# Kernel optimization log

Hardware: AMD Instinct MI355X
Metric: run time of the kernel (lower is better)

Reference implementation:

```python
import jax, jax.numpy as jnp
import numpy as np
from jax import lax

B, N, CIN, COUT, FPS, K, TCH, M, H = 8, 4096, 128, 256, 1024, 24, 256, 32, 4
HD = TCH // H
BN_SCALE = 1.0 / np.sqrt(1.0 + 1e-5)  # eval-mode BN: running_mean=0, running_var=1


def _gather(points, idx):
    # points [B,N,C], idx [B,S] or [B,S,K] -> gathered points
    return jax.vmap(lambda p, i: p[i])(points, idx)


def _bn(x, g, b):
    return x * (g * BN_SCALE) + b


def _ln(x, g, b):
    mu = jnp.mean(x, -1, keepdims=True)
    v = jnp.var(x, -1, keepdims=True)
    return (x - mu) / jnp.sqrt(v + 1e-5) * g + b


def _gelu(x):
    return jax.nn.gelu(x, approximate=False)


def _fps(xyz, npoint, farthest0):
    Bb, Nn, _ = xyz.shape
    def step(carry, _):
        dmin, far = carry
        c = jax.vmap(lambda p, i: p[i])(xyz, far)  # [B,3]
        d = jnp.sum((xyz - c[:, None, :]) ** 2, -1)
        dmin = jnp.minimum(dmin, d)
        return (dmin, jnp.argmax(dmin, -1)), far
    init = (jnp.full((Bb, Nn), 1e10, xyz.dtype), farthest0)
    _, cents = lax.scan(step, init, None, length=npoint)
    return cents.T  # [B, npoint]


def _sqdist(src, dst):
    d = -2.0 * jnp.einsum('bnc,bmc->bnm', src, dst)
    d = d + jnp.sum(src ** 2, -1)[:, :, None]
    d = d + jnp.sum(dst ** 2, -1)[:, None, :]
    return d


def _forward(xyz, x, t, farthest0, Wproj, gproj, bproj, Wl1, gl1, bl1, Wl2, gl2, bl2,
             Wc1, gc1, bc1, Wc2, gc2, bc2, Wq, Wk, Wv, Wo,
             ln1g, ln1b, Wqkv, Wao, ln2g, ln2b, Wf1, Wf2):
    # --- GenerateGraph: FPS + KNN grouping ---
    fps_idx = _fps(xyz, FPS, farthest0)            # [B,S]
    new_xyz = _gather(xyz, fps_idx)                # [B,S,3]
    xT = jnp.transpose(x, (0, 2, 1))               # [B,N,Cin]
    new_pts = _gather(xT, fps_idx)                 # [B,S,Cin]
    dist = _sqdist(new_xyz, xyz)                   # [B,S,N]
    _, idx = lax.top_k(-dist, K)                   # [B,S,K] nearest neighbors
    grouped = _gather(xT, idx)                     # [B,S,K,Cin]
    edge = grouped - new_pts[:, :, None, :]
    # --- Local: Conv1DBR proj + Conv1DBRRes (channels-last, 1x1 convs = GEMM) ---
    h = _gelu(_bn(jnp.einsum('bskc,oc->bsko', edge, Wproj), gproj, bproj))
    r = _gelu(_bn(jnp.einsum('bsko,po->bskp', h, Wl1), gl1, bl1))
    r = _bn(jnp.einsum('bskp,op->bsko', r, Wl2), gl2, bl2)
    h = _gelu(r + h)
    f = jnp.max(h, axis=2)                         # adaptive_max_pool over k -> [B,S,O]
    # --- Channel (ca): Conv1DBRRes on centroid features ---
    r = _gelu(_bn(f @ Wc1.T, gc1, bc1))
    r = _bn(r @ Wc2.T, gc2, bc2)
    f = _gelu(r + f)
    x_out = jnp.transpose(f, (0, 2, 1))            # [B,O,S]
    # --- Local2Former: tokens attend to local features ---
    q = t @ Wq.T
    kk = f @ Wk.T
    v = f @ Wv.T
    a = jax.nn.softmax(jnp.einsum('bmd,bsd->bms', q, kk) * (TCH ** -0.5), axis=-1)
    t = t + jnp.einsum('bms,bsd->bmd', a, v) @ Wo.T
    # --- Former: one pre-norm encoder layer (MHA + MLP) ---
    hn = _ln(t, ln1g, ln1b)
    qkv = (hn @ Wqkv.T).reshape(B, M, 3, H, HD).transpose(2, 0, 3, 1, 4)
    qh, kh, vh = qkv[0], qkv[1], qkv[2]            # [B,H,M,hd]
    attn = jax.nn.softmax(jnp.einsum('bhmd,bhnd->bhmn', qh, kh) * (HD ** -0.5), axis=-1)
    o = jnp.einsum('bhmn,bhnd->bhmd', attn, vh).transpose(0, 2, 1, 3).reshape(B, M, TCH)
    t = t + o @ Wao.T
    hn = _ln(t, ln2g, ln2b)
    t = t + _gelu(hn @ Wf1.T) @ Wf2.T
    return new_xyz, x_out, t


def setup_inputs() -> dict:
    key = jax.random.key(0)
    ks = jax.random.split(key, 40)
    def w(k, o, i):
        return jax.random.normal(k, (o, i), jnp.float32) / np.sqrt(i)
    def g(k, c):
        return 1.0 + 0.1 * jax.random.normal(k, (c,), jnp.float32)
    def bta(k, c):
        return 0.1 * jax.random.normal(k, (c,), jnp.float32)
    inp = {
        'xyz': jax.random.normal(ks[0], (B, N, 3), jnp.float32),
        'x': jax.random.normal(ks[1], (B, CIN, N), jnp.float32),
        't': jax.random.normal(ks[2], (B, M, TCH), jnp.float32),
        'farthest0': jax.random.randint(ks[3], (B,), 0, N),
        'Wproj': w(ks[4], COUT, CIN), 'gproj': g(ks[5], COUT), 'bproj': bta(ks[6], COUT),
        'Wl1': w(ks[7], COUT, COUT), 'gl1': g(ks[8], COUT), 'bl1': bta(ks[9], COUT),
        'Wl2': w(ks[10], COUT, COUT), 'gl2': g(ks[11], COUT), 'bl2': bta(ks[12], COUT),
        'Wc1': w(ks[13], COUT, COUT), 'gc1': g(ks[14], COUT), 'bc1': bta(ks[15], COUT),
        'Wc2': w(ks[16], COUT, COUT), 'gc2': g(ks[17], COUT), 'bc2': bta(ks[18], COUT),
        'Wq': w(ks[19], TCH, TCH), 'Wk': w(ks[20], TCH, COUT), 'Wv': w(ks[21], TCH, COUT),
        'Wo': w(ks[22], TCH, TCH),
        'ln1g': g(ks[23], TCH), 'ln1b': bta(ks[24], TCH),
        'Wqkv': w(ks[25], 3 * TCH, TCH), 'Wao': w(ks[26], TCH, TCH),
        'ln2g': g(ks[27], TCH), 'ln2b': bta(ks[28], TCH),
        'Wf1': w(ks[29], 2 * TCH, TCH), 'Wf2': w(ks[30], TCH, 2 * TCH),
    }
    return inp


def reference(xyz, x, t, farthest0, Wproj, gproj, bproj, Wl1, gl1, bl1, Wl2, gl2, bl2,
              Wc1, gc1, bc1, Wc2, gc2, bc2, Wq, Wk, Wv, Wo,
              ln1g, ln1b, Wqkv, Wao, ln2g, ln2b, Wf1, Wf2):
    return _forward(xyz, x, t, farthest0, Wproj, gproj, bproj, Wl1, gl1, bl1, Wl2, gl2, bl2,
                    Wc1, gc1, bc1, Wc2, gc2, bc2, Wq, Wk, Wv, Wo,
                    ln1g, ln1b, Wqkv, Wao, ln2g, ln2b, Wf1, Wf2)
```

## Files before the change

### kernel.cpp

```cpp
#include <hip/hip_runtime.h>
#include <math.h>

#define Bc 8
#define Nc 4096
#define CINc 128
#define COUTc 256
#define Sc 1024
#define Kc 24
#define TCHc 256
#define Mc 32
#define Hc 4
#define HDc 64
#define MBAT (Sc*Kc)

#define BN_SCALE_F 0.9999950000374997f

typedef __attribute__((ext_vector_type(8))) short bf16x8;
typedef __attribute__((ext_vector_type(4))) float f32x4;

__device__ __forceinline__ float b2f(short s){
  unsigned int u = ((unsigned int)(unsigned short)s) << 16;
  union { unsigned int u; float f; } c; c.u = u; return c.f;
}
__device__ __forceinline__ short f2b(float f){
  union { unsigned int u; float f; } c; c.f = f;
  unsigned int u = c.u;
  unsigned int r = (u + 0x7fffu + ((u >> 16) & 1u)) >> 16;
  return (short)(r & 0xffffu);
}
__device__ __forceinline__ float gelu_f(float v){
  return 0.5f * v * (1.f + erff(v * 0.7071067811865475f));
}
__device__ __forceinline__ bf16x8 ld8cvt(const short* p){ return *(const bf16x8*)p; }
__device__ __forceinline__ bf16x8 ld8cvt(const float* p){
  f32x4 a = *(const f32x4*)p; f32x4 b = *(const f32x4*)(p+4);
  bf16x8 r;
  r[0]=f2b(a[0]); r[1]=f2b(a[1]); r[2]=f2b(a[2]); r[3]=f2b(a[3]);
  r[4]=f2b(b[0]); r[5]=f2b(b[1]); r[6]=f2b(b[2]); r[7]=f2b(b[3]);
  return r;
}
__device__ __forceinline__ float rdval(const float* p){ return *p; }
__device__ __forceinline__ float rdval(const short* p){ return b2f(*p); }
__device__ __forceinline__ void wrval(float* p, float v){ *p = v; }
__device__ __forceinline__ void wrval(short* p, float v){ *p = f2b(v); }

__device__ __forceinline__ void gl_lds16(const short* g, short* l){
  __builtin_amdgcn_global_load_lds(
     (const __attribute__((address_space(1))) void*)g,
     (__attribute__((address_space(3))) void*)l, 16, 0, 0);
}

template<int CTRL>
__device__ __forceinline__ double dpp_max_f64(double v){
  long long x = __double_as_longlong(v);
  int lo = (int)(unsigned int)(x & 0xFFFFFFFFLL);
  int hi = (int)(unsigned int)((unsigned long long)x >> 32);
  int plo = __builtin_amdgcn_update_dpp(lo, lo, CTRL, 0xF, 0xF, false);
  int phi = __builtin_amdgcn_update_dpp(hi, hi, CTRL, 0xF, 0xF, false);
  double p = __longlong_as_double((long long)(((unsigned long long)(unsigned int)phi << 32)
                                              | (unsigned int)plo));
  return fmax(v, p);
}
template<int CTRL>
__device__ __forceinline__ float dpp_min_f32(float v){
  int x = __float_as_int(v);
  int p = __builtin_amdgcn_update_dpp(x, x, CTRL, 0xF, 0xF, false);
  return fminf(v, __int_as_float(p));
}
template<int CTRL>
__device__ __forceinline__ unsigned dpp_min_u32(unsigned v){
  int p = __builtin_amdgcn_update_dpp((int)v, (int)v, CTRL, 0xF, 0xF, false);
  unsigned pu = (unsigned)p;
  return v < pu ? v : pu;
}

#define PREP_FPS 8
#define PREP_TX 4096
#define PREP_CVT 64
#define PREP_DD 128
#define PREP_TOTAL (PREP_FPS+PREP_TX+PREP_CVT+PREP_DD)

__global__ __launch_bounds__(256) void prep_kernel(
    const float* __restrict__ xyz, const int* __restrict__ far0, int* __restrict__ fps_idx,
    const float* __restrict__ x, short* __restrict__ xT,
    const float* __restrict__ Wproj, const float* __restrict__ Wl1, const float* __restrict__ Wl2,
    const float* __restrict__ Wc1, const float* __restrict__ Wc2,
    const float* __restrict__ Wk, const float* __restrict__ Wv,
    short* __restrict__ wbf, float* __restrict__ dd){
  __shared__ double smem[6176];
  int bid = blockIdx.x, tid = threadIdx.x;
  if(bid < PREP_FPS){
    int b = bid;
    float* sx = (float*)smem;
    float* sy = sx + Nc;
    float* sz = sy + Nc;
    double* pwave = smem + (Nc*12)/8;
    const float* xb = xyz + (size_t)b*Nc*3;
    for(int i=tid; i<Nc; i+=256){
      const float* p = xb + i*3;
      sx[i]=p[0]; sy[i]=p[1]; sz[i]=p[2];
    }
    __syncthreads();
    float px[16], py[16], pz[16], dmin[16];
    unsigned int lokey[16];
#pragma unroll
    for(int j=0;j<16;j++){
      int n = tid + 256*j;
      px[j]=sx[n]; py[j]=sy[n]; pz[j]=sz[n];
      dmin[j]=1e10f;
      lokey[j]=(unsigned int)((Nc-1) - n);
    }
    int winner = far0[b] & (Nc-1);
    int* out = fps_idx + b*Sc;
    for(int it=0; it<Sc; it++){
      if(tid==0) out[it] = winner;
      float cx=sx[winner], cy=sy[winner], cz=sz[winner];
      double key[16];
#pragma unroll
      for(int j=0;j<16;j++){
        float dx = __fsub_rn(px[j], cx);
        float dy = __fsub_rn(py[j], cy);
        float dz = __fsub_rn(pz[j], cz);
        float d = __fadd_rn(__fadd_rn(__fmul_rn(dx,dx), __fmul_rn(dy,dy)), __fmul_rn(dz,dz));
        dmin[j] = fminf(dmin[j], d);
        unsigned long long k = (((unsigned long long)__float_as_uint(dmin[j])) << 32) | lokey[j];
        key[j] = __longlong_as_double((long long)k);
      }
#pragma unroll
      for(int st=8; st>0; st>>=1)
#pragma unroll
        for(int j=0;j<st;j++) key[j] = fmax(key[j], key[j+st]);
      double kv = key[0];
      kv = dpp_max_f64<0x111>(kv);
      kv = dpp_max_f64<0x112>(kv);
      kv = dpp_max_f64<0x114>(kv);
      kv = dpp_max_f64<0x118>(kv);
      kv = dpp_max_f64<0x142>(kv);
      kv = dpp_max_f64<0x143>(kv);
      int p = it & 1;
      if((tid & 63) == 63) pwave[p*4 + (tid>>6)] = kv;
      __syncthreads();
      double k0 = pwave[p*4+0], k1 = pwave[p*4+1], k2 = pwave[p*4+2], k3 = pwave[p*4+3];
      double kb = fmax(fmax(k0,k1), fmax(k2,k3));
      unsigned long long kbits = (unsigned long long)__double_as_longlong(kb);
      winner = (Nc-1) - (int)(kbits & 0xFFFFFFFFULL);
    }
  } else if(bid < PREP_FPS+PREP_TX){
    int t = bid - PREP_FPS;
    int b = t >> 9;
    int rem = t & 511;
    int n0 = (rem & 127) * 32;
    int c0 = (rem >> 7) * 32;
    short (*tile)[33] = (short(*)[33])smem;
    int tx = tid & 31, ty = tid >> 5;
#pragma unroll
    for(int i=0;i<32;i+=8)
      tile[ty+i][tx] = f2b(x[((size_t)b*CINc + (c0+ty+i))*Nc + n0+tx]);
    __syncthreads();
#pragma unroll
    for(int i=0;i<32;i+=8)
      xT[((size_t)b*Nc + (n0+ty+i))*CINc + c0+tx] = tile[tx][ty+i];
  } else if(bid < PREP_FPS+PREP_TX+PREP_CVT){
    int gid = (bid - PREP_FPS - PREP_TX)*256 + tid;
    const int stride = PREP_CVT*256;
    short* p = wbf;
    for(int i=gid; i<COUTc*CINc; i+=stride) p[i] = f2b(Wproj[i]);
    p += COUTc*CINc;
    for(int i=gid; i<COUTc*COUTc; i+=stride) p[i] = f2b(Wl1[i]);
    p += COUTc*COUTc;
    for(int i=gid; i<COUTc*COUTc; i+=stride) p[i] = f2b(Wl2[i]);
    p += COUTc*COUTc;
    for(int i=gid; i<COUTc*COUTc; i+=stride) p[i] = f2b(Wc1[i]);
    p += COUTc*COUTc;
    for(int i=gid; i<COUTc*COUTc; i+=stride) p[i] = f2b(Wc2[i]);
    p += COUTc*COUTc;
    for(int i=gid; i<TCHc*COUTc; i+=stride) p[i] = f2b(Wk[i]);
    p += TCHc*COUTc;
    for(int i=gid; i<TCHc*COUTc; i+=stride) p[i] = f2b(Wv[i]);
  } else {
    int i = (bid - PREP_FPS - PREP_TX - PREP_CVT)*256 + tid;
    const float* p = xyz + (size_t)i*3;
    float xx=p[0], yy=p[1], zz=p[2];
    dd[i] = __fadd_rn(__fadd_rn(__fmul_rn(xx,xx),__fmul_rn(yy,yy)),__fmul_rn(zz,zz));
  }
}

__global__ __launch_bounds__(256) void knn_kernel(const float* __restrict__ xyz,
                                                  const int* __restrict__ fps_idx,
                                                  const float* __restrict__ dd,
                                                  int* __restrict__ knn_idx,
                                                  float* __restrict__ out0){
  int bs = blockIdx.x, tid = threadIdx.x;
  int b = bs >> 10;
  __shared__ float pv[4]; __shared__ int pi[4];
  int qn = fps_idx[bs] & (Nc-1);
  const float* q = xyz + ((size_t)b*Nc + qn)*3;
  float sx = q[0], sy = q[1], sz = q[2];
  if(tid < 3) out0[bs*3 + tid] = q[tid];
  float ss = __fadd_rn(__fadd_rn(__fmul_rn(sx,sx),__fmul_rn(sy,sy)),__fmul_rn(sz,sz));
  const float* xb = xyz + (size_t)b*Nc*3;
  const float* db = dd + b*Nc;
  float dv[16];
#pragma unroll
  for(int j=0;j<16;j++){
    int n = tid + 256*j;
    float xx=xb[n*3], yy=xb[n*3+1], zz=xb[n*3+2];
    float e = __fmul_rn(sx,xx);
    e = __fadd_rn(e, __fmul_rn(sy,yy));
    e = __fadd_rn(e, __fmul_rn(sz,zz));
    dv[j] = __fadd_rn(__fadd_rn(__fmul_rn(-2.f,e), ss), db[n]);
  }
  int* ob = knn_idx + (size_t)bs*Kc;
  for(int k=0;k<Kc;k++){
    float bvv = dv[0];
#pragma unroll
    for(int j=1;j<16;j++) bvv = fminf(bvv, dv[j]);
    bvv = dpp_min_f32<0x111>(bvv);
    bvv = dpp_min_f32<0x112>(bvv);
    bvv = dpp_min_f32<0x114>(bvv);
    bvv = dpp_min_f32<0x118>(bvv);
    bvv = dpp_min_f32<0x142>(bvv);
    bvv = dpp_min_f32<0x143>(bvv);
    if((tid&63)==63) pv[tid>>6] = bvv;
    __syncthreads();
    float vmin = fminf(fminf(pv[0],pv[1]), fminf(pv[2],pv[3]));
    unsigned bi = 0xFFFFFFFFu;
#pragma unroll
    for(int j=0;j<16;j++){
      unsigned n = (unsigned)(tid + 256*j);
      if(dv[j]==vmin && n < bi) bi = n;
    }
    bi = dpp_min_u32<0x111>(bi);
    bi = dpp_min_u32<0x112>(bi);
    bi = dpp_min_u32<0x114>(bi);
    bi = dpp_min_u32<0x118>(bi);
    bi = dpp_min_u32<0x142>(bi);
    bi = dpp_min_u32<0x143>(bi);
    if((tid&63)==63) pi[tid>>6] = (int)bi;
    __syncthreads();
    unsigned i0=(unsigned)pi[0], i1=(unsigned)pi[1], i2=(unsigned)pi[2], i3=(unsigned)pi[3];
    unsigned m01 = i0<i1?i0:i1, m23 = i2<i3?i2:i3;
    unsigned win = m01<m23?m01:m23;
    if(tid==0) ob[k] = (int)(win & (Nc-1));
#pragma unroll
    for(int j=0;j<16;j++) if((int)win == tid + 256*j) dv[j] = 3.4e38f;
  }
}

template<int HAS_BN, int HAS_GELU, int HAS_RES, typename TRES>
__global__ __launch_bounds__(256) void gemm128(
    const short* __restrict__ A, const short* __restrict__ W,
    const float* __restrict__ g, const float* __restrict__ bias,
    const TRES* __restrict__ Res, short* __restrict__ Out,
    int Nn, int Kk){
  __shared__ short As[128*32];
  __shared__ short Bs[128*32];
  int bm = blockIdx.y*128, bn = blockIdx.x*128;
  int tid = threadIdx.x;
  int wave = tid>>6, lane = tid&63, quad = lane>>4, l16 = lane&15;
  int wr = (wave>>1)*64, wc = (wave&1)*64;
  f32x4 acc[4][4];
#pragma unroll
  for(int i=0;i<4;i++)
#pragma unroll
    for(int j=0;j<4;j++) acc[i][j] = (f32x4){0.f,0.f,0.f,0.f};
  int sr = tid>>2, scc = (tid&3)*8;
  const short* Ap = A + (size_t)(bm+sr)*Kk + scc;
  const short* Wp = W + (size_t)(bn+sr)*Kk + scc;
  for(int k0=0; k0<Kk; k0+=32){
    gl_lds16(Ap + k0,                    As + tid*8);
    gl_lds16(Ap + k0 + (size_t)64*Kk,    As + 2048 + tid*8);
    gl_lds16(Wp + k0,                    Bs + tid*8);
    gl_lds16(Wp + k0 + (size_t)64*Kk,    Bs + 2048 + tid*8);
    __syncthreads();
    bf16x8 af[4], bfr[4];
#pragma unroll
    for(int mt=0; mt<4; mt++) af[mt]  = *(const bf16x8*)&As[(wr+mt*16+l16)*32 + quad*8];
#pragma unroll
    for(int nt=0; nt<4; nt++) bfr[nt] = *(const bf16x8*)&Bs[(wc+nt*16+l16)*32 + quad*8];
#pragma unroll
    for(int mt=0; mt<4; mt++)
#pragma unroll
      for(int nt=0; nt<4; nt++)
        acc[mt][nt] = __builtin_amdgcn_mfma_f32_16x16x32_bf16(af[mt], bfr[nt], acc[mt][nt], 0, 0, 0);
    __syncthreads();
  }
#pragma unroll
  for(int nt=0; nt<4; nt++){
    int col = bn + wc + nt*16 + l16;
    float gs = 0.f, bs_ = 0.f;
    if(HAS_BN){ gs = g[col] * BN_SCALE_F; bs_ = bias[col]; }
#pragma unroll
    for(int mt=0; mt<4; mt++){
#pragma unroll
      for(int r2=0;r2<4;r2++){
        int row = bm + wr + mt*16 + quad*4 + r2;
        float v = acc[mt][nt][r2];
        if(HAS_BN) v = v*gs + bs_;
        if(HAS_RES) v += rdval(Res + (size_t)row*Nn + col);
        if(HAS_GELU) v = gelu_f(v);
        Out[(size_t)row*Nn + col] = f2b(v);
      }
    }
  }
}

__global__ __launch_bounds__(256) void proj128(
    const short* __restrict__ xT, const int* __restrict__ knn_idx, const int* __restrict__ fps_idx,
    const short* __restrict__ W, const float* __restrict__ g, const float* __restrict__ bias,
    short* __restrict__ Out){
  __shared__ short As[128*32];
  __shared__ short Bs[128*32];
  int bm = blockIdx.y*128, bn = blockIdx.x*128;
  int tid = threadIdx.x;
  int wave = tid>>6, lane = tid&63, quad = lane>>4, l16 = lane&15;
  int wr = (wave>>1)*64, wc = (wave&1)*64;
  f32x4 acc[4][4];
#pragma unroll
  for(int i=0;i<4;i++)
#pragma unroll
    for(int j=0;j<4;j++) acc[i][j] = (f32x4){0.f,0.f,0.f,0.f};
  int sr = tid>>2, scc = (tid&3)*8;
  int R0 = bm + sr, R1 = R0 + 64;
  int b0 = R0 / (Sc*Kc), b1 = R1 / (Sc*Kc);
  int nk0 = knn_idx[R0] & (Nc-1), nk1 = knn_idx[R1] & (Nc-1);
  int nc0 = fps_idx[R0 / Kc] & (Nc-1), nc1 = fps_idx[R1 / Kc] & (Nc-1);
  const short* pk0 = xT + ((size_t)b0*Nc + nk0)*CINc + scc;
  const short* pc0 = xT + ((size_t)b0*Nc + nc0)*CINc + scc;
  const short* pk1 = xT + ((size_t)b1*Nc + nk1)*CINc + scc;
  const short* pc1 = xT + ((size_t)b1*Nc + nc1)*CINc + scc;
  const short* Wp  = W + (size_t)(bn+sr)*CINc + scc;
  for(int k0=0; k0<CINc; k0+=32){
    gl_lds16(Wp + k0,                      Bs + tid*8);
    gl_lds16(Wp + k0 + (size_t)64*CINc,    Bs + 2048 + tid*8);
    bf16x8 vk = *(const bf16x8*)(pk0 + k0);
    bf16x8 vc = *(const bf16x8*)(pc0 + k0);
    bf16x8 e0, e1;
#pragma unroll
    for(int i=0;i<8;i++) e0[i] = f2b(__fsub_rn(b2f(vk[i]), b2f(vc[i])));
    vk = *(const bf16x8*)(pk1 + k0);
    vc = *(const bf16x8*)(pc1 + k0);
#pragma unroll
    for(int i=0;i<8;i++) e1[i] = f2b(__fsub_rn(b2f(vk[i]), b2f(vc[i])));
    *(bf16x8*)&As[tid*8] = e0;
    *(bf16x8*)&As[2048 + tid*8] = e1;
    __syncthreads();
    bf16x8 af[4], bfr[4];
#pragma unroll
    for(int mt=0; mt<4; mt++) af[mt]  = *(const bf16x8*)&As[(wr+mt*16+l16)*32 + quad*8];
#pragma unroll
    for(int nt=0; nt<4; nt++) bfr[nt] = *(const bf16x8*)&Bs[(wc+nt*16+l16)*32 + quad*8];
#pragma unroll
    for(int mt=0; mt<4; mt++)
#pragma unroll
      for(int nt=0; nt<4; nt++)
        acc[mt][nt] = __builtin_amdgcn_mfma_f32_16x16x32_bf16(af[mt], bfr[nt], acc[mt][nt], 0, 0, 0);
    __syncthreads();
  }
#pragma unroll
  for(int nt=0; nt<4; nt++){
    int col = bn + wc + nt*16 + l16;
    float gs = g[col] * BN_SCALE_F, bs_ = bias[col];
#pragma unroll
    for(int mt=0; mt<4; mt++){
#pragma unroll
      for(int r2=0;r2<4;r2++){
        int row = bm + wr + mt*16 + quad*4 + r2;
        float v = acc[mt][nt][r2]*gs + bs_;
        Out[(size_t)row*COUTc + col] = f2b(gelu_f(v));
      }
    }
  }
}

template<int HAS_BN, int HAS_GELU, int HAS_RES, typename TRES, typename TOUT>
__global__ __launch_bounds__(256) void gemm64d(
    const short* __restrict__ A, const short* __restrict__ W,
    const float* __restrict__ g, const float* __restrict__ bias,
    const TRES* __restrict__ Res, TOUT* __restrict__ Out,
    int Nn, int Kk){
  __shared__ short As[64*32];
  __shared__ short Bs[64*32];
  int bm = blockIdx.y*64, bn = blockIdx.x*64;
  int tid = threadIdx.x;
  int wave = tid >> 6, lane = tid & 63, quad = lane >> 4, l16 = lane & 15;
  f32x4 acc[4];
#pragma unroll
  for(int i=0;i<4;i++) acc[i] = (f32x4){0.f,0.f,0.f,0.f};
  const short* Ap = A + (size_t)(bm + (tid>>2))*Kk + (tid&3)*8;
  const short* Wp = W + (size_t)(bn + (tid>>2))*Kk + (tid&3)*8;
  for(int k0=0; k0<Kk; k0+=32){
    gl_lds16(Ap + k0, As + tid*8);
    gl_lds16(Wp + k0, Bs + tid*8);
    __syncthreads();
    bf16x8 a = *(const bf16x8*)&As[(wave*16 + l16)*32 + quad*8];
#pragma unroll
    for(int ct=0; ct<4; ct++){
      bf16x8 bb = *(const bf16x8*)&Bs[(ct*16 + l16)*32 + quad*8];
      acc[ct] = __builtin_amdgcn_mfma_f32_16x16x32_bf16(a, bb, acc[ct], 0, 0, 0);
    }
    __syncthreads();
  }
#pragma unroll
  for(int ct=0; ct<4; ct++){
    int col = bn + ct*16 + l16;
    float gs = 0.f, bs_ = 0.f;
    if(HAS_BN){ gs = g[col] * BN_SCALE_F; bs_ = bias[col]; }
#pragma unroll
    for(int r2=0;r2<4;r2++){
      int row = bm + wave*16 + quad*4 + r2;
      float v = acc[ct][r2];
      if(HAS_BN) v = v*gs + bs_;
      if(HAS_RES) v += rdval(Res + (size_t)row*Nn + col);
      if(HAS_GELU) v = gelu_f(v);
      wrval(Out + (size_t)row*Nn + col, v);
    }
  }
}

__global__ __launch_bounds__(192) void gemm_l2max(
    const short* __restrict__ A, const short* __restrict__ W,
    const float* __restrict__ g, const float* __restrict__ bias,
    const short* __restrict__ Hres, short* __restrict__ Fout, int R0){
  __shared__ short As[48*32];
  __shared__ short Bs[64*32];
  __shared__ float sm[48][65];
  int bm = blockIdx.y*48, bn = blockIdx.x*64;
  int tid = threadIdx.x;
  int wave = tid >> 6, lane = tid & 63, quad = lane >> 4, l16 = lane & 15;
  f32x4 acc[4];
#pragma unroll
  for(int i=0;i<4;i++) acc[i] = (f32x4){0.f,0.f,0.f,0.f};
  const short* Ap  = A + (size_t)(bm + (tid>>2))*COUTc + (tid&3)*8;
  const short* Wp  = W + (size_t)(bn + (tid>>2))*COUTc + (tid&3)*8;
  const short* Wp2 = W + (size_t)(bn + 48 + (lane>>2))*COUTc + (lane&3)*8;
  for(int k0=0; k0<COUTc; k0+=32){
    gl_lds16(Ap + k0, As + tid*8);
    gl_lds16(Wp + k0, Bs + tid*8);
    if(wave==0) gl_lds16(Wp2 + k0, Bs + 1536 + lane*8);
    __syncthreads();
    bf16x8 a = *(const bf16x8*)&As[(wave*16 + l16)*32 + quad*8];
#pragma unroll
    for(int ct=0; ct<4; ct++){
      bf16x8 bb = *(const bf16x8*)&Bs[(ct*16 + l16)*32 + quad*8];
      acc[ct] = __builtin_amdgcn_mfma_f32_16x16x32_bf16(a, bb, acc[ct], 0, 0, 0);
    }
    __syncthreads();
  }
#pragma unroll
  for(int ct=0; ct<4; ct++){
    int col = bn + ct*16 + l16;
    float gs = g[col] * BN_SCALE_F, bs_ = bias[col];
#pragma unroll
    for(int r2=0;r2<4;r2++){
      int rl = wave*16 + quad*4 + r2;
      float v = acc[ct][r2]*gs + bs_;
      v += b2f(Hres[(size_t)(bm+rl)*COUTc + col]);
      sm[rl][ct*16 + l16] = gelu_f(v);
    }
  }
  __syncthreads();
  if(tid < 128){
    int gl = tid >> 6, col = tid & 63;
    float mx = -3.4e38f;
#pragma unroll
    for(int kk=0; kk<Kc; kk++) mx = fmaxf(mx, sm[gl*Kc + kk][col]);
    int gg = R0/Kc + blockIdx.y*2 + gl;
    Fout[(size_t)gg*COUTc + bn + col] = f2b(mx);
  }
}

template<typename TA, typename TRES, typename TOUT, int HAS_BN, int HAS_GELU, int HAS_RES>
__global__ __launch_bounds__(256) void gemm_bf16(
    const TA* __restrict__ A, const float* __restrict__ W,
    const float* __restrict__ g, const float* __restrict__ bias,
    const TRES* __restrict__ Res, TOUT* __restrict__ Out,
    int Nn, int Kk){
  __shared__ short As[64][40];
  __shared__ short Bs[64][40];
  int bm = blockIdx.y*64, bn = blockIdx.x*64;
  int tid = threadIdx.x;
  int wave = tid >> 6, lane = tid & 63, quad = lane >> 4, l16 = lane & 15;
  f32x4 acc[4];
#pragma unroll
  for(int i=0;i<4;i++) acc[i] = (f32x4){0.f,0.f,0.f,0.f};
  int ar = tid >> 2, ac = (tid & 3) * 8;
  const TA*    Ap = A + (size_t)(bm + ar)*Kk + ac;
  const float* Wp = W + (size_t)(bn + ar)*Kk + ac;
  for(int k0=0; k0<Kk; k0+=32){
    *(bf16x8*)&As[ar][ac] = ld8cvt(Ap + k0);
    *(bf16x8*)&Bs[ar][ac] = ld8cvt(Wp + k0);
    __syncthreads();
    bf16x8 a = *(const bf16x8*)&As[wave*16 + l16][quad*8];
#pragma unroll
    for(int ct=0; ct<4; ct++){
      bf16x8 bb = *(const bf16x8*)&Bs[ct*16 + l16][quad*8];
      acc[ct] = __builtin_amdgcn_mfma_f32_16x16x32_bf16(a, bb, acc[ct], 0, 0, 0);
    }
    __syncthreads();
  }
#pragma unroll
  for(int ct=0; ct<4; ct++){
    int col = bn + ct*16 + l16;
    float gs = 0.f, bs_ = 0.f;
    if(HAS_BN){ gs = g[col] * BN_SCALE_F; bs_ = bias[col]; }
#pragma unroll
    for(int r2=0;r2<4;r2++){
      int row = bm + wave*16 + quad*4 + r2;
      float v = acc[ct][r2];
      if(HAS_BN) v = v*gs + bs_;
      if(HAS_RES) v += rdval(Res + (size_t)row*Nn + col);
      if(HAS_GELU) v = gelu_f(v);
      wrval(Out + (size_t)row*Nn + col, v);
    }
  }
}

__global__ __launch_bounds__(256) void transpose_f(const short* __restrict__ f2, float* __restrict__ out1){
  __shared__ short tile[32][33];
  int b = blockIdx.z;
  int s0 = blockIdx.x*32, c0 = blockIdx.y*32;
  int tx = threadIdx.x & 31, ty = threadIdx.x >> 5;
#pragma unroll
  for(int i=0;i<32;i+=8)
    tile[ty+i][tx] = f2[((size_t)b*Sc + (s0+ty+i))*COUTc + c0+tx];
  __syncthreads();
#pragma unroll
  for(int i=0;i<32;i+=8)
    out1[((size_t)b*COUTc + (c0+ty+i))*Sc + s0+tx] = b2f(tile[tx][ty+i]);
}

__global__ __launch_bounds__(256) void l2f_attn(
    const short* __restrict__ qb, const short* __restrict__ kv,
    short* __restrict__ ao){
  int blk = blockIdx.x; int b = blk / Mc; int m = blk % Mc;
  int tid = threadIdx.x;
  __shared__ float qs[TCHc];
  __shared__ float aw[Sc];
  __shared__ float red[8];
  qs[tid] = b2f(qb[(size_t)(b*Mc+m)*TCHc + tid]);
  __syncthreads();
  float sc[4];
#pragma unroll
  for(int jj=0;jj<4;jj++){
    int j = tid + 256*jj;
    const short* kp = kv + ((size_t)b*Sc + j)*512;
    float a = 0.f;
    for(int c=0;c<TCHc;c+=8){
      bf16x8 v8 = *(const bf16x8*)(kp + c);
#pragma unroll
      for(int i=0;i<8;i++) a += b2f(v8[i]) * qs[c+i];
    }
    sc[jj] = a * 0.0625f;
  }
  float mx = fmaxf(fmaxf(sc[0],sc[1]), fmaxf(sc[2],sc[3]));
#pragma unroll
  for(int off=32; off>0; off>>=1) mx = fmaxf(mx, __shfl_xor(mx, off));
  if((tid&63)==0) red[tid>>6] = mx;
  __syncthreads();
  mx = fmaxf(fmaxf(red[0],red[1]), fmaxf(red[2],red[3]));
  float se = 0.f;
#pragma unroll
  for(int jj=0;jj<4;jj++){
    float e = expf(sc[jj] - mx);
    aw[tid + 256*jj] = e;
    se += e;
  }
#pragma unroll
  for(int off=32; off>0; off>>=1) se += __shfl_xor(se, off);
  if((tid&63)==0) red[4 + (tid>>6)] = se;
  __syncthreads();
  se = red[4]+red[5]+red[6]+red[7];
  float inv = 1.f/se;
#pragma unroll
  for(int jj=0;jj<4;jj++) aw[tid + 256*jj] *= inv;
  __syncthreads();
  float acc = 0.f;
  const short* vp = kv + (size_t)b*Sc*512 + 256 + tid;
  for(int j=0;j<Sc;j++) acc += aw[j] * b2f(vp[(size_t)j*512]);
  ao[(size_t)(b*Mc+m)*TCHc + tid] = f2b(acc);
}

__global__ __launch_bounds__(64) void former_attn(const short* __restrict__ qkv, short* __restrict__ oa){
  int blk = blockIdx.x;
  int m = blk % Mc; int bh = blk / Mc; int h = bh % Hc; int b = bh / Hc;
  int lane = threadIdx.x;
  __shared__ float qs[HDc];
  __shared__ float aw2[32];
  const short* base = qkv + (size_t)(b*Mc)*(3*TCHc);
  qs[lane] = b2f(base[(size_t)m*3*TCHc + h*HDc + lane]);
  __syncthreads();
  int j = lane & 31;
  const short* kp = base + (size_t)j*3*TCHc + TCHc + h*HDc;
  float s = 0.f;
  for(int d=0; d<HDc; d+=8){
    bf16x8 v8 = *(const bf16x8*)(kp + d);
#pragma unroll
    for(int i=0;i<8;i++) s += b2f(v8[i]) * qs[d+i];
  }
  s *= 0.125f;
  float mx = s;
#pragma unroll
  for(int off=16; off>0; off>>=1) mx = fmaxf(mx, __shfl_xor(mx, off, 32));
  float e = expf(s - mx);
  float se = e;
#pragma unroll
  for(int off=16; off>0; off>>=1) se += __shfl_xor(se, off, 32);
  if(lane < 32) aw2[lane] = e / se;
  __syncthreads();
  float acc = 0.f;
  const short* vp = base + 2*TCHc + h*HDc + lane;
  for(int jj=0; jj<32; jj++) acc += aw2[jj] * b2f(vp[(size_t)jj*3*TCHc]);
  oa[(size_t)(b*Mc+m)*TCHc + h*HDc + lane] = f2b(acc);
}

__global__ __launch_bounds__(64) void ln_kernel(const float* __restrict__ X, const float* __restrict__ g,
                                                const float* __restrict__ bb, short* __restrict__ O){
  int row = blockIdx.x, lane = threadIdx.x;
  const float* xp = X + (size_t)row*TCHc;
  float x[4];
#pragma unroll
  for(int j2=0;j2<4;j2++) x[j2] = xp[lane + 64*j2];
  float sm = x[0]+x[1]+x[2]+x[3];
#pragma unroll
  for(int off=32; off>0; off>>=1) sm += __shfl_xor(sm, off);
  float mu = sm * (1.f/256.f);
  float vs = 0.f;
#pragma unroll
  for(int j2=0;j2<4;j2++){ float d = x[j2]-mu; vs += d*d; }
#pragma unroll
  for(int off=32; off>0; off>>=1) vs += __shfl_xor(vs, off);
  float var = vs * (1.f/256.f);
  float rstd = 1.f / sqrtf(var + 1e-5f);
#pragma unroll
  for(int j2=0;j2<4;j2++){
    int c = lane + 64*j2;
    float o = (x[j2]-mu)*rstd*g[c] + bb[c];
    O[(size_t)row*TCHc + c] = f2b(o);
  }
}

extern "C" void kernel_launch(void* const* d_in, const int* in_sizes, int n_in,
                              void* d_out, int out_size, void* d_ws, size_t ws_size,
                              hipStream_t stream){
  const float* xyz  = (const float*)d_in[0];
  const float* x    = (const float*)d_in[1];
  const float* t_in = (const float*)d_in[2];
  const int*   far0 = (const int*)d_in[3];
  const float* Wproj=(const float*)d_in[4];  const float* gproj=(const float*)d_in[5];  const float* bproj=(const float*)d_in[6];
  const float* Wl1 = (const float*)d_in[7];  const float* gl1 = (const float*)d_in[8];  const float* bl1 = (const float*)d_in[9];
  const float* Wl2 = (const float*)d_in[10]; const float* gl2 = (const float*)d_in[11]; const float* bl2 = (const float*)d_in[12];
  const float* Wc1 = (const float*)d_in[13]; const float* gc1 = (const float*)d_in[14]; const float* bc1 = (const float*)d_in[15];
  const float* Wc2 = (const float*)d_in[16]; const float* gc2 = (const float*)d_in[17]; const float* bc2 = (const float*)d_in[18];
  const float* Wq  = (const float*)d_in[19]; const float* Wk  = (const float*)d_in[20]; const float* Wv  = (const float*)d_in[21];
  const float* Wo  = (const float*)d_in[22];
  const float* ln1g= (const float*)d_in[23]; const float* ln1b= (const float*)d_in[24];
  const float* Wqkv= (const float*)d_in[25]; const float* Wao = (const float*)d_in[26];
  const float* ln2g= (const float*)d_in[27]; const float* ln2b= (const float*)d_in[28];
  const float* Wf1 = (const float*)d_in[29]; const float* Wf2 = (const float*)d_in[30];

  char* wsb = (char*)d_ws;
  size_t off = 0;
  auto alloc = [&](size_t bytes)->void*{ void* p = wsb + off; off += (bytes + 255) & ~(size_t)255; return p; };
  int*   fps_i = (int*)alloc((size_t)Bc*Sc*4);
  float* ddb   = (float*)alloc((size_t)Bc*Nc*4);
  int*   knn   = (int*)alloc((size_t)Bc*Sc*Kc*4);
  short* xT    = (short*)alloc((size_t)Bc*Nc*CINc*2);
  short* wbf   = (short*)alloc((size_t)(COUTc*CINc + 4*COUTc*COUTc + 2*TCHc*COUTc)*2);
  short* fbuf  = (short*)alloc((size_t)Bc*Sc*COUTc*2);
  short* rcbuf = (short*)alloc((size_t)Bc*Sc*COUTc*2);
  short* f2buf = (short*)alloc((size_t)Bc*Sc*COUTc*2);
  short* kvbuf = (short*)alloc((size_t)Bc*Sc*512*2);
  short* qbuf  = (short*)alloc((size_t)Bc*Mc*TCHc*2);
  short* a1out = (short*)alloc((size_t)Bc*Mc*TCHc*2);
  float* t1buf = (float*)alloc((size_t)Bc*Mc*TCHc*4);
  short* hnbuf = (short*)alloc((size_t)Bc*Mc*TCHc*2);
  short* qkvb  = (short*)alloc((size_t)Bc*Mc*3*TCHc*2);
  short* a2out = (short*)alloc((size_t)Bc*Mc*TCHc*2);
  float* t2buf = (float*)alloc((size_t)Bc*Mc*TCHc*4);
  short* hn2buf= (short*)alloc((size_t)Bc*Mc*TCHc*2);
  short* g1buf = (short*)alloc((size_t)Bc*Mc*2*TCHc*2);
  size_t full_bytes  = (size_t)Bc*MBAT*COUTc*2;
  size_t batch_bytes = (size_t)MBAT*COUTc*2;
  bool batched = (off + 2*(full_bytes + 256) <= ws_size);
  short* hbuf = (short*)alloc(batched ? full_bytes : batch_bytes);
  short* rbuf = (short*)alloc(batched ? full_bytes : batch_bytes);
  if(off > ws_size) return;

  short* wproj_bf = wbf;
  short* wl1_bf   = wproj_bf + COUTc*CINc;
  short* wl2_bf   = wl1_bf + COUTc*COUTc;
  short* wc1_bf   = wl2_bf + COUTc*COUTc;
  short* wc2_bf   = wc1_bf + COUTc*COUTc;
  short* wkv_bf   = wc2_bf + COUTc*COUTc;

  float* out0 = (float*)d_out;
  float* out1 = out0 + (size_t)Bc*Sc*3;
  float* out2 = out1 + (size_t)Bc*COUTc*Sc;

  prep_kernel<<<PREP_TOTAL, 256, 0, stream>>>(xyz, far0, fps_i, x, xT,
                                              Wproj, Wl1, Wl2, Wc1, Wc2, Wk, Wv, wbf, ddb);
  knn_kernel<<<Bc*Sc, 256, 0, stream>>>(xyz, fps_i, ddb, knn, out0);
  if(batched){
    proj128<<<dim3(COUTc/128, (Bc*MBAT)/128), 256, 0, stream>>>(xT, knn, fps_i, wproj_bf, gproj, bproj, hbuf);
    gemm128<1,1,0,short><<<dim3(COUTc/128, (Bc*MBAT)/128), 256, 0, stream>>>(hbuf, wl1_bf, gl1, bl1, (const short*)nullptr, rbuf, COUTc, COUTc);
    gemm_l2max<<<dim3(COUTc/64, (Bc*MBAT)/48), 192, 0, stream>>>(rbuf, wl2_bf, gl2, bl2, hbuf, fbuf, 0);
  } else {
    for(int b=0; b<Bc; b++){
      gemm64d<0,0,0,short,short><<<dim3(1,1), 256, 0, stream>>>(nullptr, nullptr, nullptr, nullptr, (const short*)nullptr, (short*)nullptr, 0, 0);
    }
  }
  gemm64d<1,1,0,short,short><<<dim3(COUTc/64, (Bc*Sc)/64), 256, 0, stream>>>(fbuf, wc1_bf, gc1, bc1, (const short*)nullptr, rcbuf, COUTc, COUTc);
  gemm64d<1,1,1,short,short><<<dim3(COUTc/64, (Bc*Sc)/64), 256, 0, stream>>>(rcbuf, wc2_bf, gc2, bc2, fbuf, f2buf, COUTc, COUTc);
  transpose_f<<<dim3(Sc/32, COUTc/32, Bc), 256, 0, stream>>>(f2buf, out1);
  gemm_bf16<float,short,short,0,0,0><<<dim3(TCHc/64, (Bc*Mc)/64), 256, 0, stream>>>(t_in, Wq, nullptr, nullptr, (const short*)nullptr, qbuf, TCHc, TCHc);
  gemm64d<0,0,0,short,short><<<dim3(512/64, (Bc*Sc)/64), 256, 0, stream>>>(f2buf, wkv_bf, nullptr, nullptr, (const short*)nullptr, kvbuf, 512, COUTc);
  l2f_attn<<<Bc*Mc, 256, 0, stream>>>(qbuf, kvbuf, a1out);
  gemm_bf16<short,float,float,0,0,1><<<dim3(TCHc/64, (Bc*Mc)/64), 256, 0, stream>>>(a1out, Wo, nullptr, nullptr, t_in, t1buf, TCHc, TCHc);
  ln_kernel<<<Bc*Mc, 64, 0, stream>>>(t1buf, ln1g, ln1b, hnbuf);
  gemm_bf16<short,short,short,0,0,0><<<dim3((3*TCHc)/64, (Bc*Mc)/64), 256, 0, stream>>>(hnbuf, Wqkv, nullptr, nullptr, (const short*)nullptr, qkvb, 3*TCHc, TCHc);
  former_attn<<<Bc*Hc*Mc, 64, 0, stream>>>(qkvb, a2out);
  gemm_bf16<short,float,float,0,0,1><<<dim3(TCHc/64, (Bc*Mc)/64), 256, 0, stream>>>(a2out, Wao, nullptr, nullptr, t1buf, t2buf, TCHc, TCHc);
  ln_kernel<<<Bc*Mc, 64, 0, stream>>>(t2buf, ln2g, ln2b, hn2buf);
  gemm_bf16<short,short,short,0,1,0><<<dim3((2*TCHc)/64, (Bc*Mc)/64), 256, 0, stream>>>(hn2buf, Wf1, nullptr, nullptr, (const short*)nullptr, g1buf, 2*TCHc, TCHc);
  gemm_bf16<short,float,float,0,0,1><<<dim3(TCHc/64, (Bc*Mc)/64), 256, 0, stream>>>(g1buf, Wf2, nullptr, nullptr, t2buf, out2, TCHc, 2*TCHc);
}
```

Before: 1.252 ms.

## Widen FPS block to 512 threads, enlarge L2+max GEMM tile, fill fallback path

```diff
diff --git a/kernel.cpp b/kernel.cpp
--- a/kernel.cpp
+++ b/kernel.cpp
@@ -73,14 +73,18 @@
   unsigned pu = (unsigned)p;
   return v < pu ? v : pu;
 }
+__device__ __forceinline__ double packkey(float d, unsigned lo){
+  unsigned long long k = (((unsigned long long)__float_as_uint(d)) << 32) | lo;
+  return __longlong_as_double((long long)k);
+}
 
 #define PREP_FPS 8
 #define PREP_TX 4096
 #define PREP_CVT 64
-#define PREP_DD 128
+#define PREP_DD 64
 #define PREP_TOTAL (PREP_FPS+PREP_TX+PREP_CVT+PREP_DD)
 
-__global__ __launch_bounds__(256) void prep_kernel(
+__global__ __launch_bounds__(512) void prep_kernel(
     const float* __restrict__ xyz, const int* __restrict__ far0, int* __restrict__ fps_idx,
     const float* __restrict__ x, short* __restrict__ xT,
     const float* __restrict__ Wproj, const float* __restrict__ Wl1, const float* __restrict__ Wl2,
@@ -94,43 +98,39 @@
     float* sx = (float*)smem;
     float* sy = sx + Nc;
     float* sz = sy + Nc;
-    double* pwave = smem + (Nc*12)/8;
+    double* pwave = smem + 6144;
     const float* xb = xyz + (size_t)b*Nc*3;
-    for(int i=tid; i<Nc; i+=256){
+    for(int i=tid; i<Nc; i+=512){
       const float* p = xb + i*3;
       sx[i]=p[0]; sy[i]=p[1]; sz[i]=p[2];
     }
     __syncthreads();
-    float px[16], py[16], pz[16], dmin[16];
-    unsigned int lokey[16];
-#pragma unroll
-    for(int j=0;j<16;j++){
-      int n = tid + 256*j;
+    float px[8], py[8], pz[8];
+    double key[8];
+    unsigned int lokey[8];
+#pragma unroll
+    for(int j=0;j<8;j++){
+      int n = tid + 512*j;
       px[j]=sx[n]; py[j]=sy[n]; pz[j]=sz[n];
-      dmin[j]=1e10f;
       lokey[j]=(unsigned int)((Nc-1) - n);
+      key[j]=packkey(1e10f, lokey[j]);
     }
     int winner = far0[b] & (Nc-1);
     int* out = fps_idx + b*Sc;
     for(int it=0; it<Sc; it++){
       if(tid==0) out[it] = winner;
       float cx=sx[winner], cy=sy[winner], cz=sz[winner];
-      double key[16];
-#pragma unroll
-      for(int j=0;j<16;j++){
+#pragma unroll
+      for(int j=0;j<8;j++){
         float dx = __fsub_rn(px[j], cx);
         float dy = __fsub_rn(py[j], cy);
         float dz = __fsub_rn(pz[j], cz);
         float d = __fadd_rn(__fadd_rn(__fmul_rn(dx,dx), __fmul_rn(dy,dy)), __fmul_rn(dz,dz));
-        dmin[j] = fminf(dmin[j], d);
-        unsigned long long k = (((unsigned long long)__float_as_uint(dmin[j])) << 32) | lokey[j];
-        key[j] = __longlong_as_double((long long)k);
+        key[j] = fmin(key[j], packkey(d, lokey[j]));
       }
-#pragma unroll
-      for(int st=8; st>0; st>>=1)
-#pragma unroll
-        for(int j=0;j<st;j++) key[j] = fmax(key[j], key[j+st]);
-      double kv = key[0];
+      double t0 = fmax(key[0],key[1]), t1 = fmax(key[2],key[3]);
+      double t2 = fmax(key[4],key[5]), t3 = fmax(key[6],key[7]);
+      double kv = fmax(fmax(t0,t1), fmax(t2,t3));
       kv = dpp_max_f64<0x111>(kv);
       kv = dpp_max_f64<0x112>(kv);
       kv = dpp_max_f64<0x114>(kv);
@@ -138,10 +138,13 @@
       kv = dpp_max_f64<0x142>(kv);
       kv = dpp_max_f64<0x143>(kv);
       int p = it & 1;
-      if((tid & 63) == 63) pwave[p*4 + (tid>>6)] = kv;
+      if((tid & 63) == 63) pwave[p*8 + (tid>>6)] = kv;
       __syncthreads();
-      double k0 = pwave[p*4+0], k1 = pwave[p*4+1], k2 = pwave[p*4+2], k3 = pwave[p*4+3];
-      double kb = fmax(fmax(k0,k1), fmax(k2,k3));
+      double m0 = fmax(pwave[p*8+0], pwave[p*8+1]);
+      double m1 = fmax(pwave[p*8+2], pwave[p*8+3]);
+      double m2 = fmax(pwave[p*8+4], pwave[p*8+5]);
+      double m3 = fmax(pwave[p*8+6], pwave[p*8+7]);
+      double kb = fmax(fmax(m0,m1), fmax(m2,m3));
       unsigned long long kbits = (unsigned long long)__double_as_longlong(kb);
       winner = (Nc-1) - (int)(kbits & 0xFFFFFFFFULL);
     }
@@ -154,15 +157,15 @@
     short (*tile)[33] = (short(*)[33])smem;
     int tx = tid & 31, ty = tid >> 5;
 #pragma unroll
-    for(int i=0;i<32;i+=8)
+    for(int i=0;i<32;i+=16)
       tile[ty+i][tx] = f2b(x[((size_t)b*CINc + (c0+ty+i))*Nc + n0+tx]);
     __syncthreads();
 #pragma unroll
-    for(int i=0;i<32;i+=8)
+    for(int i=0;i<32;i+=16)
       xT[((size_t)b*Nc + (n0+ty+i))*CINc + c0+tx] = tile[tx][ty+i];
   } else if(bid < PREP_FPS+PREP_TX+PREP_CVT){
-    int gid = (bid - PREP_FPS - PREP_TX)*256 + tid;
-    const int stride = PREP_CVT*256;
+    int gid = (bid - PREP_FPS - PREP_TX)*512 + tid;
+    const int stride = PREP_CVT*512;
     short* p = wbf;
     for(int i=gid; i<COUTc*CINc; i+=stride) p[i] = f2b(Wproj[i]);
     p += COUTc*CINc;
@@ -178,7 +181,7 @@
     p += TCHc*COUTc;
     for(int i=gid; i<TCHc*COUTc; i+=stride) p[i] = f2b(Wv[i]);
   } else {
-    int i = (bid - PREP_FPS - PREP_TX - PREP_CVT)*256 + tid;
+    int i = (bid - PREP_FPS - PREP_TX - PREP_CVT)*512 + tid;
     const float* p = xyz + (size_t)i*3;
     float xx=p[0], yy=p[1], zz=p[2];
     dd[i] = __fadd_rn(__fadd_rn(__fmul_rn(xx,xx),__fmul_rn(yy,yy)),__fmul_rn(zz,zz));
@@ -308,7 +311,7 @@
 __global__ __launch_bounds__(256) void proj128(
     const short* __restrict__ xT, const int* __restrict__ knn_idx, const int* __restrict__ fps_idx,
     const short* __restrict__ W, const float* __restrict__ g, const float* __restrict__ bias,
-    short* __restrict__ Out){
+    short* __restrict__ Out, int R0){
   __shared__ short As[128*32];
   __shared__ short Bs[128*32];
   int bm = blockIdx.y*128, bn = blockIdx.x*128;
@@ -321,10 +324,10 @@
 #pragma unroll
     for(int j=0;j<4;j++) acc[i][j] = (f32x4){0.f,0.f,0.f,0.f};
   int sr = tid>>2, scc = (tid&3)*8;
-  int R0 = bm + sr, R1 = R0 + 64;
-  int b0 = R0 / (Sc*Kc), b1 = R1 / (Sc*Kc);
-  int nk0 = knn_idx[R0] & (Nc-1), nk1 = knn_idx[R1] & (Nc-1);
-  int nc0 = fps_idx[R0 / Kc] & (Nc-1), nc1 = fps_idx[R1 / Kc] & (Nc-1);
+  int Rg0 = R0 + bm + sr, Rg1 = Rg0 + 64;
+  int b0 = Rg0 / (Sc*Kc), b1 = Rg1 / (Sc*Kc);
+  int nk0 = knn_idx[Rg0] & (Nc-1), nk1 = knn_idx[Rg1] & (Nc-1);
+  int nc0 = fps_idx[Rg0 / Kc] & (Nc-1), nc1 = fps_idx[Rg1 / Kc] & (Nc-1);
   const short* pk0 = xT + ((size_t)b0*Nc + nk0)*CINc + scc;
   const short* pc0 = xT + ((size_t)b0*Nc + nc0)*CINc + scc;
   const short* pk1 = xT + ((size_t)b1*Nc + nk1)*CINc + scc;
@@ -370,6 +373,72 @@
         Out[(size_t)row*COUTc + col] = f2b(gelu_f(v));
       }
     }
+  }
+}
+
+__global__ __launch_bounds__(256) void l2max96(
+    const short* __restrict__ A, const short* __restrict__ W,
+    const float* __restrict__ g, const float* __restrict__ bias,
+    const short* __restrict__ Hres, short* __restrict__ Fout, int R0){
+  __shared__ __align__(16) char sbuf[96*129*4];
+  short* As = (short*)sbuf;
+  short* Bs = (short*)(sbuf + 6144);
+  float (*sm)[129] = (float(*)[129])sbuf;
+  int bm = blockIdx.y*96, bn = blockIdx.x*128;
+  int tid = threadIdx.x;
+  int wave = tid>>6, lane = tid&63, quad = lane>>4, l16 = lane&15;
+  int wr = (wave>>1)*48, wc = (wave&1)*64;
+  f32x4 acc[3][4];
+#pragma unroll
+  for(int i=0;i<3;i++)
+#pragma unroll
+    for(int j=0;j<4;j++) acc[i][j] = (f32x4){0.f,0.f,0.f,0.f};
+  int sr = tid>>2, scc = (tid&3)*8;
+  const short* Ap = A + (size_t)(bm+sr)*COUTc + scc;
+  const short* Wp = W + (size_t)(bn+sr)*COUTc + scc;
+  for(int k0=0; k0<COUTc; k0+=32){
+    gl_lds16(Ap + k0, As + tid*8);
+    if(tid < 128) gl_lds16(Ap + k0 + (size_t)64*COUTc, As + 2048 + tid*8);
+    gl_lds16(Wp + k0, Bs + tid*8);
+    gl_lds16(Wp + k0 + (size_t)64*COUTc, Bs + 2048 + tid*8);
+    __syncthreads();
+    bf16x8 af[3], bfr[4];
+#pragma unroll
+    for(int mt=0; mt<3; mt++) af[mt]  = *(const bf16x8*)&As[(wr+mt*16+l16)*32 + quad*8];
+#pragma unroll
+    for(int nt=0; nt<4; nt++) bfr[nt] = *(const bf16x8*)&Bs[(wc+nt*16+l16)*32 + quad*8];
+#pragma unroll
+    for(int mt=0; mt<3; mt++)
+#pragma unroll
+      for(int nt=0; nt<4; nt++)
+        acc[mt][nt] = __builtin_amdgcn_mfma_f32_16x16x32_bf16(af[mt], bfr[nt], acc[mt][nt], 0, 0, 0);
+    __syncthreads();
+  }
+#pragma unroll
+  for(int nt=0; nt<4; nt++){
+    int col = bn + wc + nt*16 + l16;
+    float gs = g[col] * BN_SCALE_F, bs_ = bias[col];
+#pragma unroll
+    for(int mt=0; mt<3; mt++){
+#pragma unroll
+      for(int r2=0;r2<4;r2++){
+        int rl = wr + mt*16 + quad*4 + r2;
+        float v = acc[mt][nt][r2]*gs + bs_;
+        v += b2f(Hres[(size_t)(bm+rl)*COUTc + col]);
+        sm[rl][wc + nt*16 + l16] = gelu_f(v);
+      }
+    }
+  }
+  __syncthreads();
+#pragma unroll
+  for(int rep=0; rep<2; rep++){
+    int idx = rep*256 + tid;
+    int gg = idx >> 7, col = idx & 127;
+    float mx = -3.4e38f;
+#pragma unroll
+    for(int kk=0; kk<Kc; kk++) mx = fmaxf(mx, sm[gg*Kc + kk][col]);
+    int srow = R0/Kc + blockIdx.y*4 + gg;
+    Fout[(size_t)srow*COUTc + bn + col] = f2b(mx);
   }
 }
 
@@ -415,58 +484,6 @@
       if(HAS_GELU) v = gelu_f(v);
       wrval(Out + (size_t)row*Nn + col, v);
     }
-  }
-}
-
-__global__ __launch_bounds__(192) void gemm_l2max(
-    const short* __restrict__ A, const short* __restrict__ W,
-    const float* __restrict__ g, const float* __restrict__ bias,
-    const short* __restrict__ Hres, short* __restrict__ Fout, int R0){
-  __shared__ short As[48*32];
-  __shared__ short Bs[64*32];
-  __shared__ float sm[48][65];
-  int bm = blockIdx.y*48, bn = blockIdx.x*64;
-  int tid = threadIdx.x;
-  int wave = tid >> 6, lane = tid & 63, quad = lane >> 4, l16 = lane & 15;
-  f32x4 acc[4];
-#pragma unroll
-  for(int i=0;i<4;i++) acc[i] = (f32x4){0.f,0.f,0.f,0.f};
-  const short* Ap  = A + (size_t)(bm + (tid>>2))*COUTc + (tid&3)*8;
-  const short* Wp  = W + (size_t)(bn + (tid>>2))*COUTc + (tid&3)*8;
-  const short* Wp2 = W + (size_t)(bn + 48 + (lane>>2))*COUTc + (lane&3)*8;
-  for(int k0=0; k0<COUTc; k0+=32){
-    gl_lds16(Ap + k0, As + tid*8);
-    gl_lds16(Wp + k0, Bs + tid*8);
-    if(wave==0) gl_lds16(Wp2 + k0, Bs + 1536 + lane*8);
-    __syncthreads();
-    bf16x8 a = *(const bf16x8*)&As[(wave*16 + l16)*32 + quad*8];
-#pragma unroll
-    for(int ct=0; ct<4; ct++){
-      bf16x8 bb = *(const bf16x8*)&Bs[(ct*16 + l16)*32 + quad*8];
-      acc[ct] = __builtin_amdgcn_mfma_f32_16x16x32_bf16(a, bb, acc[ct], 0, 0, 0);
-    }
-    __syncthreads();
-  }
-#pragma unroll
-  for(int ct=0; ct<4; ct++){
-    int col = bn + ct*16 + l16;
-    float gs = g[col] * BN_SCALE_F, bs_ = bias[col];
-#pragma unroll
-    for(int r2=0;r2<4;r2++){
-      int rl = wave*16 + quad*4 + r2;
-      float v = acc[ct][r2]*gs + bs_;
-      v += b2f(Hres[(size_t)(bm+rl)*COUTc + col]);
-      sm[rl][ct*16 + l16] = gelu_f(v);
-    }
-  }
-  __syncthreads();
-  if(tid < 128){
-    int gl = tid >> 6, col = tid & 63;
-    float mx = -3.4e38f;
-#pragma unroll
-    for(int kk=0; kk<Kc; kk++) mx = fmaxf(mx, sm[gl*Kc + kk][col]);
-    int gg = R0/Kc + blockIdx.y*2 + gl;
-    Fout[(size_t)gg*COUTc + bn + col] = f2b(mx);
   }
 }
 
@@ -698,16 +715,18 @@
   float* out1 = out0 + (size_t)Bc*Sc*3;
   float* out2 = out1 + (size_t)Bc*COUTc*Sc;
 
-  prep_kernel<<<PREP_TOTAL, 256, 0, stream>>>(xyz, far0, fps_i, x, xT,
+  prep_kernel<<<PREP_TOTAL, 512, 0, stream>>>(xyz, far0, fps_i, x, xT,
                                               Wproj, Wl1, Wl2, Wc1, Wc2, Wk, Wv, wbf, ddb);
   knn_kernel<<<Bc*Sc, 256, 0, stream>>>(xyz, fps_i, ddb, knn, out0);
   if(batched){
-    proj128<<<dim3(COUTc/128, (Bc*MBAT)/128), 256, 0, stream>>>(xT, knn, fps_i, wproj_bf, gproj, bproj, hbuf);
+    proj128<<<dim3(COUTc/128, (Bc*MBAT)/128), 256, 0, stream>>>(xT, knn, fps_i, wproj_bf, gproj, bproj, hbuf, 0);
     gemm128<1,1,0,short><<<dim3(COUTc/128, (Bc*MBAT)/128), 256, 0, stream>>>(hbuf, wl1_bf, gl1, bl1, (const short*)nullptr, rbuf, COUTc, COUTc);
-    gemm_l2max<<<dim3(COUTc/64, (Bc*MBAT)/48), 192, 0, stream>>>(rbuf, wl2_bf, gl2, bl2, hbuf, fbuf, 0);
+    l2max96<<<dim3(COUTc/128, (Bc*MBAT)/96), 256, 0, stream>>>(rbuf, wl2_bf, gl2, bl2, hbuf, fbuf, 0);
   } else {
     for(int b=0; b<Bc; b++){
-      gemm64d<0,0,0,short,short><<<dim3(1,1), 256, 0, stream>>>(nullptr, nullptr, nullptr, nullptr, (const short*)nullptr, (short*)nullptr, 0, 0);
+      proj128<<<dim3(COUTc/128, MBAT/128), 256, 0, stream>>>(xT, knn, fps_i, wproj_bf, gproj, bproj, hbuf, b*MBAT);
+      gemm128<1,1,0,short><<<dim3(COUTc/128, MBAT/128), 256, 0, stream>>>(hbuf, wl1_bf, gl1, bl1, (const short*)nullptr, rbuf, COUTc, COUTc);
+      l2max96<<<dim3(COUTc/128, MBAT/96), 256, 0, stream>>>(rbuf, wl2_bf, gl2, bl2, hbuf, fbuf, b*MBAT);
     }
   }
   gemm64d<1,1,0,short,short><<<dim3(COUTc/64, (Bc*Sc)/64), 256, 0, stream>>>(fbuf, wc1_bf, gc1, bc1, (const short*)nullptr, rcbuf, COUTc, COUTc);
```

Result: slower. 1.335 ms (+6.6%).
